# Kernel optimization log

Hardware: AMD Instinct MI355X
Metric: run time of the kernel (lower is better)

Reference implementation:

```python
import jax, jax.numpy as jnp
import numpy as np

B, S, H, NH = 2, 2048, 2048, 16
HD = H // NH  # 128
ROPE_BASE = 10000.0


def _rope(q, k, position_ids):
    # q, k: [B, NH, S, HD]; position_ids: [B, S]
    half = HD // 2
    inv_freq = 1.0 / (ROPE_BASE ** (jnp.arange(0, half, dtype=jnp.float32) / half))
    freqs = position_ids.astype(jnp.float32)[:, :, None] * inv_freq[None, None, :]  # [B,S,half]
    emb = jnp.concatenate([freqs, freqs], axis=-1)                                   # [B,S,HD]
    cos = jnp.cos(emb)[:, None, :, :]  # [B,1,S,HD]
    sin = jnp.sin(emb)[:, None, :, :]

    def rot_half(x):
        x1, x2 = jnp.split(x, 2, axis=-1)
        return jnp.concatenate([-x2, x1], axis=-1)

    q = q * cos + rot_half(q) * sin
    k = k * cos + rot_half(k) * sin
    return q, k


def setup_inputs() -> dict:
    key = jax.random.key(0)
    k1, k2, k3 = jax.random.split(key, 3)
    hidden_states = jax.random.normal(k1, (B, S, H), dtype=jnp.float32)
    position_ids = jnp.broadcast_to(jnp.arange(S, dtype=jnp.int32), (B, S))
    # additive causal mask (large finite negative to avoid inf arithmetic)
    causal = jnp.triu(jnp.full((S, S), -1e9, dtype=jnp.float32), k=1)
    attention_mask = jnp.broadcast_to(causal[None, None], (B, 1, S, S))
    qkv_w = jax.random.normal(k2, (3 * H, H), dtype=jnp.float32) * (H ** -0.5)
    qkv_b = jnp.zeros((3 * H,), dtype=jnp.float32)
    o_w = jax.random.normal(k3, (H, H), dtype=jnp.float32) * (H ** -0.5)
    return {"hidden_states": hidden_states, "position_ids": position_ids,
            "attention_mask": attention_mask, "qkv_w": qkv_w, "qkv_b": qkv_b, "o_w": o_w}


def reference(hidden_states, position_ids, attention_mask, qkv_w, qkv_b, o_w):
    qkv = hidden_states @ qkv_w.T + qkv_b                      # [B,S,3H]
    q, k, v = jnp.split(qkv, 3, axis=-1)

    def to_heads(x):
        return x.reshape(B, S, NH, HD).transpose(0, 2, 1, 3)   # [B,NH,S,HD]

    q, k, v = to_heads(q), to_heads(k), to_heads(v)
    q, k = _rope(q, k, position_ids)

    scale = 1.0 / np.sqrt(HD)
    scores = jnp.einsum('bhqd,bhkd->bhqk', q, k * scale)
    scores = scores + attention_mask
    probs = jax.nn.softmax(scores.astype(jnp.float32), axis=-1).astype(q.dtype)
    attn = jnp.einsum('bhqk,bhkd->bhqd', probs, v)
    attn = attn.transpose(0, 2, 1, 3).reshape(B, S, H)
    return attn @ o_w.T
```

## Files before the change

kernel.cpp:

```cpp
#include <hip/hip_runtime.h>
#include <hip/hip_bf16.h>

#define BB 2
#define SS 2048
#define HH 2048
#define NHH 16
#define HDD 128

using f32x4  = __attribute__((ext_vector_type(4))) float;
using bf16x8 = __attribute__((ext_vector_type(8))) short;

__device__ __forceinline__ unsigned short f2bf(float x) {
  unsigned int u = __float_as_uint(x);
  unsigned int r = (u + 0x7FFFu + ((u >> 16) & 1u)) >> 16;
  return (unsigned short)r;
}
__device__ __forceinline__ float bf2f(unsigned short u) {
  return __uint_as_float(((unsigned int)u) << 16);
}

__device__ __forceinline__ void gll16(const void* g, void* l) {
  __builtin_amdgcn_global_load_lds(
      (__attribute__((address_space(1))) void*)(g),
      (__attribute__((address_space(3))) void*)(l), 16, 0, 0);
}

#define MFMA16(a, b, c) __builtin_amdgcn_mfma_f32_16x16x32_bf16(a, b, c, 0, 0, 0)


__global__ void convert_bf16(const float* __restrict__ in, unsigned short* __restrict__ out, int n4) {
  int i = blockIdx.x * blockDim.x + threadIdx.x;
  if (i >= n4) return;
  float4 v = reinterpret_cast<const float4*>(in)[i];
  ushort4 o;
  o.x = f2bf(v.x); o.y = f2bf(v.y); o.z = f2bf(v.z); o.w = f2bf(v.w);
  reinterpret_cast<ushort4*>(out)[i] = o;
}

__global__ void build_tab(float* __restrict__ tab) {
  int i = blockIdx.x * blockDim.x + threadIdx.x;
  if (i >= SS * 64) return;
  int s = i >> 6, j = i & 63;
  float invf = expf(-logf(10000.f) * ((float)j / 64.f));
  float a = (float)s * invf;
  tab[i * 2]     = cosf(a);
  tab[i * 2 + 1] = sinf(a);
}


template<int MODE, int MI>
__global__ __launch_bounds__(512, 1)
void gemm_pipe(const unsigned short* __restrict__ A,
               const unsigned short* __restrict__ Bw,
               const float* __restrict__ bias,
               float* __restrict__ outF,
               unsigned short* __restrict__ outQ,
               unsigned short* __restrict__ outK,
               unsigned short* __restrict__ outV,
               int Kdim) {
  constexpr int BM = 32 * MI;
  __shared__ unsigned short lA[2][BM * 64];
  __shared__ unsigned short lB[2][256 * 64];
  const int tid = threadIdx.x;
  const int tn = blockIdx.x, tm = blockIdx.y;
  const int wid = tid >> 6, lane = tid & 63;
  const int wm = wid >> 2, wn = wid & 3;
  const int lr = lane & 15, lg = lane >> 4;

  const unsigned short* Ab = A + (size_t)tm * BM * Kdim;
  const unsigned short* Bb = Bw + (size_t)tn * 256 * Kdim;

  f32x4 acc[MI][4] = {};
  bf16x8 af[MI][2], bfr[4][2];

  const int nt = Kdim >> 6;

  auto stageA = [&](int t, int h) {
    unsigned short* L = lA[t & 1];
    const int k0 = t << 6;
#pragma unroll
    for (int p = 0; p < BM / 128; ++p) {
      int cl = p * 512 + tid;
      int ri = cl >> 3, c = cl & 7;
      int row = (ri / (8 * MI)) * (16 * MI) + h * (8 * MI) + (ri % (8 * MI));
      int cg = c ^ (row & 7);
      gll16(Ab + (size_t)row * Kdim + k0 + (cg << 3), L + row * 64 + (c << 3));
    }
  };
  auto stageB = [&](int t, int h) {
    unsigned short* L = lB[t & 1];
    const int k0 = t << 6;
#pragma unroll
    for (int p = 0; p < 2; ++p) {
      int cl = p * 512 + tid;
      int ri = cl >> 3, c = cl & 7;
      int row = (ri >> 5 << 6) + (h << 5) + (ri & 31);
      int cg = c ^ (row & 7);
      gll16(Bb + (size_t)row * Kdim + k0 + (cg << 3), L + row * 64 + (c << 3));
    }
  };
  auto readAhalf = [&](int g, int h) {
    const unsigned short* la = lA[g & 1];
#pragma unroll
    for (int mi = h * (MI / 2); mi < (h + 1) * (MI / 2); ++mi) {
      int ra = wm * (BM / 2) + mi * 16 + lr;
      af[mi][0] = *reinterpret_cast<const bf16x8*>(la + ra * 64 + ((lg ^ (ra & 7)) << 3));
      af[mi][1] = *reinterpret_cast<const bf16x8*>(la + ra * 64 + (((4 + lg) ^ (ra & 7)) << 3));
    }
  };
  auto readBhalf = [&](int g, int h) {
    const unsigned short* lb = lB[g & 1];
#pragma unroll
    for (int ni = h * 2; ni < h * 2 + 2; ++ni) {
      int rb = wn * 64 + ni * 16 + lr;
      bfr[ni][0] = *reinterpret_cast<const bf16x8*>(lb + rb * 64 + ((lg ^ (rb & 7)) << 3));
      bfr[ni][1] = *reinterpret_cast<const bf16x8*>(lb + rb * 64 + (((4 + lg) ^ (rb & 7)) << 3));
    }
  };
  auto quad = [&](int ah, int bh) {
    __builtin_amdgcn_s_setprio(1);
#pragma unroll
    for (int mi = ah * (MI / 2); mi < (ah + 1) * (MI / 2); ++mi)
#pragma unroll
      for (int ni = bh * 2; ni < bh * 2 + 2; ++ni) {
        acc[mi][ni] = MFMA16(af[mi][0], bfr[ni][0], acc[mi][ni]);
        acc[mi][ni] = MFMA16(af[mi][1], bfr[ni][1], acc[mi][ni]);
      }
    __builtin_amdgcn_s_setprio(0);
  };

  stageA(0, 0); stageA(0, 1); stageB(0, 0); stageB(0, 1);
  stageA(1, 0); stageA(1, 1); stageB(1, 0); stageB(1, 1);
  if constexpr (MI == 8) asm volatile("s_waitcnt vmcnt(8)" ::: "memory");
  else                   asm volatile("s_waitcnt vmcnt(6)" ::: "memory");
  __builtin_amdgcn_s_barrier();
  __builtin_amdgcn_sched_barrier(0);
  readAhalf(0, 0);
  readBhalf(0, 0);

  for (int g = 0; g < nt; ++g) {
    readBhalf(g, 1);
    asm volatile("s_waitcnt lgkmcnt(4)" ::: "memory");
    __builtin_amdgcn_sched_barrier(0);
    quad(0, 0);

    readAhalf(g, 1);
    if constexpr (MI == 8) asm volatile("s_waitcnt lgkmcnt(8)" ::: "memory");
    else                   asm volatile("s_waitcnt lgkmcnt(4)" ::: "memory");
    __builtin_amdgcn_sched_barrier(0);
    quad(0, 1);

    asm volatile("s_waitcnt vmcnt(0) lgkmcnt(0)" ::: "memory");
    __builtin_amdgcn_s_barrier();
    __builtin_amdgcn_sched_barrier(0);
    if (g + 1 < nt) readAhalf(g + 1, 0);
    if (g + 2 < nt) { stageA(g + 2, 0); stageA(g + 2, 1); }
    quad(1, 0);

    if (g + 1 < nt) readBhalf(g + 1, 0);
    if (g + 2 < nt) { stageB(g + 2, 0); stageB(g + 2, 1); }
    quad(1, 1);
  }

#pragma unroll
  for (int mi = 0; mi < MI; ++mi) {
#pragma unroll
    for (int ni = 0; ni < 4; ++ni) {
      int n = tn * 256 + wn * 64 + ni * 16 + lr;
#pragma unroll
      for (int r = 0; r < 4; ++r) {
        int m = tm * BM + wm * (BM / 2) + mi * 16 + lg * 4 + r;
        float v = acc[mi][ni][r];
        if (MODE == 1) {
          v += bias[n];
          int sel = n >> 11;
          int h = (n >> 7) & 15;
          int d = n & 127;
          int b = m >> 11;
          int s = m & 2047;
          if (sel == 0)
            outQ[(((size_t)(b * 16 + h)) * 2048 + s) * 128 + d] = f2bf(v);
          else if (sel == 1)
            outK[(((size_t)(b * 16 + h)) * 2048 + s) * 128 + d] = f2bf(v);
          else
            outV[(((size_t)(b * 16 + h)) * 128 + d) * 2048 + s] = f2bf(v);
        } else {
          outF[(size_t)m * 2048 + n] = v;
        }
      }
    }
  }
}


__global__ void rope_inplace(unsigned short* __restrict__ Qr, unsigned short* __restrict__ Kr,
                             const int* __restrict__ pos, const float* __restrict__ tab) {
  int i = blockIdx.x * blockDim.x + threadIdx.x;
  if (i >= (1 << 20)) return;
  int jb = i & 7;
  int s  = (i >> 3) & 2047;
  int bh = (i >> 14) & 31;
  int a  = i >> 19;
  unsigned short* base = (a ? Kr : Qr) + (((size_t)bh * 2048 + s) * 128);
  int b = bh >> 4;
  int p = pos[b * 2048 + s];
  bf16x8 x1 = *reinterpret_cast<bf16x8*>(base + jb * 8);
  bf16x8 x2 = *reinterpret_cast<bf16x8*>(base + 64 + jb * 8);
  bf16x8 y1, y2;
#pragma unroll
  for (int t = 0; t < 8; ++t) {
    int j = jb * 8 + t;
    float c  = tab[((size_t)p * 64 + j) * 2];
    float sn = tab[((size_t)p * 64 + j) * 2 + 1];
    float a1 = bf2f((unsigned short)x1[t]);
    float a2 = bf2f((unsigned short)x2[t]);
    y1[t] = (short)f2bf(a1 * c - a2 * sn);
    y2[t] = (short)f2bf(a2 * c + a1 * sn);
  }
  *reinterpret_cast<bf16x8*>(base + jb * 8) = y1;
  *reinterpret_cast<bf16x8*>(base + 64 + jb * 8) = y2;
}


__global__ __launch_bounds__(256)
void attn_fwd(const unsigned short* __restrict__ Qr,
              const unsigned short* __restrict__ Kr,
              const unsigned short* __restrict__ Vt,
              unsigned short* __restrict__ attnb) {
  __shared__ unsigned short Ks[64 * 128];
  __shared__ unsigned short Vs[128 * 64];
  __shared__ unsigned short Ps[64 * 64];
  const int bx = blockIdx.x, bh = blockIdx.y;
  const int tid = threadIdx.x;
  const int wid = tid >> 6, lane = tid & 63;
  const int lr = lane & 15, lg = lane >> 4;
  const unsigned short* Qb = Qr + (size_t)bh * SS * HDD;
  const unsigned short* Kb = Kr + (size_t)bh * SS * HDD;
  const unsigned short* Vb = Vt + (size_t)bh * HDD * SS;
  const int b = bh >> 4, h = bh & 15;

#pragma unroll 1
  for (int qi = 0; qi < 2; ++qi) {
    const int qt = qi ? bx : (31 - bx);

    bf16x8 qf[4];
#pragma unroll
    for (int kk = 0; kk < 4; ++kk)
      qf[kk] = *reinterpret_cast<const bf16x8*>(
          Qb + ((size_t)(qt * 64 + wid * 16 + lr)) * 128 + kk * 32 + lg * 8);

    f32x4 oacc[8] = {};
    float mrow[4], lsum[4];
#pragma unroll
    for (int r = 0; r < 4; ++r) { mrow[r] = -1e30f; lsum[r] = 0.f; }

    for (int kt = 0; kt <= qt; ++kt) {
#pragma unroll
      for (int ch = 0; ch < 4; ++ch) {
        int c = tid + ch * 256;
        {
          int row = c >> 4, cb = c & 15;
          gll16(Kb + ((size_t)(kt * 64 + row)) * 128 + ((cb ^ (row & 7)) << 3), Ks + c * 8);
        }
        {
          int row = c >> 3, cb = c & 7;
          gll16(Vb + (size_t)row * SS + kt * 64 + ((cb ^ (row & 7)) << 3), Vs + c * 8);
        }
      }
      __syncthreads();

      float sv[4][4];
#pragma unroll
      for (int nt = 0; nt < 4; ++nt) {
        f32x4 sa = {};
#pragma unroll
        for (int kk = 0; kk < 4; ++kk) {
          int row = nt * 16 + lr;
          bf16x8 kf = *reinterpret_cast<const bf16x8*>(
              Ks + row * 128 + (((kk * 4 + lg) ^ (row & 7)) << 3));
          sa = __builtin_amdgcn_mfma_f32_16x16x32_bf16(qf[kk], kf, sa, 0, 0, 0);
        }
#pragma unroll
        for (int r = 0; r < 4; ++r) {
          float s = sa[r] * 0.088388347648318447f;
          if (kt == qt && (nt * 16 + lr) > (wid * 16 + lg * 4 + r)) s -= 1e9f;
          sv[nt][r] = s;
        }
      }

      float tmax[4];
#pragma unroll
      for (int r = 0; r < 4; ++r)
        tmax[r] = fmaxf(fmaxf(sv[0][r], sv[1][r]), fmaxf(sv[2][r], sv[3][r]));
#pragma unroll
      for (int r = 0; r < 4; ++r) {
        tmax[r] = fmaxf(tmax[r], __shfl_xor(tmax[r], 1));
        tmax[r] = fmaxf(tmax[r], __shfl_xor(tmax[r], 2));
        tmax[r] = fmaxf(tmax[r], __shfl_xor(tmax[r], 4));
        tmax[r] = fmaxf(tmax[r], __shfl_xor(tmax[r], 8));
      }
      float fr[4], tsum[4];
#pragma unroll
      for (int r = 0; r < 4; ++r) {
        float mn = fmaxf(mrow[r], tmax[r]);
        fr[r] = __expf(mrow[r] - mn);
        mrow[r] = mn;
        tsum[r] = 0.f;
      }
#pragma unroll
      for (int nt = 0; nt < 4; ++nt) {
        int colc = nt * 2 + (lr >> 3);
#pragma unroll
        for (int r = 0; r < 4; ++r) {
          float p = __expf(sv[nt][r] - mrow[r]);
          tsum[r] += p;
          int row = wid * 16 + lg * 4 + r;
          Ps[row * 64 + ((colc ^ (row & 7)) << 3) + (lr & 7)] = f2bf(p);
        }
      }
#pragma unroll
      for (int r = 0; r < 4; ++r) {
        tsum[r] += __shfl_xor(tsum[r], 1);
        tsum[r] += __shfl_xor(tsum[r], 2);
        tsum[r] += __shfl_xor(tsum[r], 4);
        tsum[r] += __shfl_xor(tsum[r], 8);
        lsum[r] = lsum[r] * fr[r] + tsum[r];
      }
#pragma unroll
      for (int ct = 0; ct < 8; ++ct)
#pragma unroll
        for (int r = 0; r < 4; ++r)
          oacc[ct][r] *= fr[r];

      bf16x8 pf[2];
#pragma unroll
      for (int ks = 0; ks < 2; ++ks) {
        int row = wid * 16 + lr;
        pf[ks] = *reinterpret_cast<const bf16x8*>(
            Ps + row * 64 + (((ks * 4 + lg) ^ (row & 7)) << 3));
      }
#pragma unroll
      for (int ct = 0; ct < 8; ++ct) {
#pragma unroll
        for (int ks = 0; ks < 2; ++ks) {
          int row = ct * 16 + lr;
          bf16x8 vf = *reinterpret_cast<const bf16x8*>(
              Vs + row * 64 + (((ks * 4 + lg) ^ (row & 7)) << 3));
          oacc[ct] = __builtin_amdgcn_mfma_f32_16x16x32_bf16(pf[ks], vf, oacc[ct], 0, 0, 0);
        }
      }
      __syncthreads();
    }

#pragma unroll
    for (int r = 0; r < 4; ++r) {
      float rl = 1.f / lsum[r];
      int qg = qt * 64 + wid * 16 + lg * 4 + r;
#pragma unroll
      for (int ct = 0; ct < 8; ++ct) {
        int d = ct * 16 + lr;
        attnb[((size_t)b * SS + qg) * HH + h * 128 + d] = f2bf(oacc[ct][r] * rl);
      }
    }
  }
}


extern "C" void kernel_launch(void* const* d_in, const int* in_sizes, int n_in,
                              void* d_out, int out_size, void* d_ws, size_t ws_size,
                              hipStream_t stream) {
  const float* hs     = (const float*)d_in[0];
  const int*   pos    = (const int*)d_in[1];
  const float* qkv_w  = (const float*)d_in[3];
  const float* qkv_b  = (const float*)d_in[4];
  const float* o_w    = (const float*)d_in[5];
  float* out = (float*)d_out;
  char* ws = (char*)d_ws;

  unsigned short* hsb   = (unsigned short*)(ws);
  unsigned short* wqkvb = (unsigned short*)(ws + 16777216);
  unsigned short* owb   = (unsigned short*)(ws + 41943040);
  unsigned short* Qr    = (unsigned short*)(ws + 50331648);
  unsigned short* Kr    = (unsigned short*)(ws + 67108864);
  unsigned short* Vt    = (unsigned short*)(ws + 83886080);
  unsigned short* attnb = (unsigned short*)(ws + 100663296);
  float*          tab   = (float*)(ws + 117440512);

  convert_bf16<<<2097152 / 256, 256, 0, stream>>>(hs, hsb, 2097152);
  convert_bf16<<<3145728 / 256, 256, 0, stream>>>(qkv_w, wqkvb, 3145728);
  convert_bf16<<<1048576 / 256, 256, 0, stream>>>(o_w, owb, 1048576);
  build_tab<<<512, 256, 0, stream>>>(tab);

  gemm_pipe<1, 8><<<dim3(24, 16), 512, 0, stream>>>(hsb, wqkvb, qkv_b, nullptr, Qr, Kr, Vt, 2048);
  rope_inplace<<<4096, 256, 0, stream>>>(Qr, Kr, pos, tab);
  attn_fwd<<<dim3(16, 32), 256, 0, stream>>>(Qr, Kr, Vt, attnb);
  gemm_pipe<0, 4><<<dim3(8, 32), 512, 0, stream>>>(attnb, owb, nullptr, out, nullptr, nullptr, nullptr, 2048);
}
```

Measured before the change: 318.7 us.

## Parametrize GEMM N-tile width and double-buffer K/V tiles in attention

The GEMM kernel gains an NB template parameter so the QKV projection can use 192-wide N tiles. That gives 32x16=512 blocks instead of 24x16=384, which should fill the CUs more evenly; the wait counts and the MFMA/read interleave are regenerated per column fragment. The attention kernel now double-buffers its K and V LDS tiles, issuing the next tile's global-to-LDS loads before computing on the current one, with explicit vmcnt waits and raw barriers in place of __syncthreads. This doubles the attention kernel's K/V LDS footprint, and the hand-tuned waitcnt values depend on the exact number of loads issued per thread.

```diff
diff --git a/kernel.cpp b/kernel.cpp
--- a/kernel.cpp
+++ b/kernel.cpp
@@ -26,6 +26,26 @@
 }
 
 #define MFMA16(a, b, c) __builtin_amdgcn_mfma_f32_16x16x32_bf16(a, b, c, 0, 0, 0)
+
+template<int N> __device__ __forceinline__ void wlgkm() {
+  static_assert(N == 0 || N == 2 || N == 4 || N == 6 || N == 8 || N == 10 || N == 12,
+                "unsupported lgkmcnt");
+  if constexpr (N == 0)       asm volatile("s_waitcnt lgkmcnt(0)"  ::: "memory");
+  else if constexpr (N == 2)  asm volatile("s_waitcnt lgkmcnt(2)"  ::: "memory");
+  else if constexpr (N == 4)  asm volatile("s_waitcnt lgkmcnt(4)"  ::: "memory");
+  else if constexpr (N == 6)  asm volatile("s_waitcnt lgkmcnt(6)"  ::: "memory");
+  else if constexpr (N == 8)  asm volatile("s_waitcnt lgkmcnt(8)"  ::: "memory");
+  else if constexpr (N == 10) asm volatile("s_waitcnt lgkmcnt(10)" ::: "memory");
+  else if constexpr (N == 12) asm volatile("s_waitcnt lgkmcnt(12)" ::: "memory");
+}
+template<int N> __device__ __forceinline__ void wvm() {
+  static_assert(N == 0 || N == 5 || N == 6 || N == 7 || N == 8, "unsupported vmcnt");
+  if constexpr (N == 0)      asm volatile("s_waitcnt vmcnt(0)" ::: "memory");
+  else if constexpr (N == 5) asm volatile("s_waitcnt vmcnt(5)" ::: "memory");
+  else if constexpr (N == 6) asm volatile("s_waitcnt vmcnt(6)" ::: "memory");
+  else if constexpr (N == 7) asm volatile("s_waitcnt vmcnt(7)" ::: "memory");
+  else if constexpr (N == 8) asm volatile("s_waitcnt vmcnt(8)" ::: "memory");
+}
 
 
 __global__ void convert_bf16(const float* __restrict__ in, unsigned short* __restrict__ out, int n4) {
@@ -48,7 +68,7 @@
 }
 
 
-template<int MODE, int MI>
+template<int MODE, int MI, int NB>
 __global__ __launch_bounds__(512, 1)
 void gemm_pipe(const unsigned short* __restrict__ A,
                const unsigned short* __restrict__ Bw,
@@ -59,8 +79,10 @@
                unsigned short* __restrict__ outV,
                int Kdim) {
   constexpr int BM = 32 * MI;
+  constexpr int BN = 64 * NB;
+  constexpr int TOPS = 2 * (BM / 128) + NB;
   __shared__ unsigned short lA[2][BM * 64];
-  __shared__ unsigned short lB[2][256 * 64];
+  __shared__ unsigned short lB[2][BN * 64];
   const int tid = threadIdx.x;
   const int tn = blockIdx.x, tm = blockIdx.y;
   const int wid = tid >> 6, lane = tid & 63;
@@ -68,10 +90,10 @@
   const int lr = lane & 15, lg = lane >> 4;
 
   const unsigned short* Ab = A + (size_t)tm * BM * Kdim;
-  const unsigned short* Bb = Bw + (size_t)tn * 256 * Kdim;
-
-  f32x4 acc[MI][4] = {};
-  bf16x8 af[MI][2], bfr[4][2];
+  const unsigned short* Bb = Bw + (size_t)tn * BN * Kdim;
+
+  f32x4 acc[MI][NB] = {};
+  bf16x8 af[MI][2], bfr[NB][2];
 
   const int nt = Kdim >> 6;
 
@@ -90,14 +112,11 @@
   auto stageB = [&](int t, int h) {
     unsigned short* L = lB[t & 1];
     const int k0 = t << 6;
-#pragma unroll
-    for (int p = 0; p < 2; ++p) {
-      int cl = p * 512 + tid;
-      int ri = cl >> 3, c = cl & 7;
-      int row = (ri >> 5 << 6) + (h << 5) + (ri & 31);
-      int cg = c ^ (row & 7);
-      gll16(Bb + (size_t)row * Kdim + k0 + (cg << 3), L + row * 64 + (c << 3));
-    }
+    int cl = tid;
+    int ri = cl >> 3, c = cl & 7;
+    int row = (ri >> 4) * (16 * NB) + h * 16 + (ri & 15);
+    int cg = c ^ (row & 7);
+    gll16(Bb + (size_t)row * Kdim + k0 + (cg << 3), L + row * 64 + (c << 3));
   };
   auto readAhalf = [&](int g, int h) {
     const unsigned short* la = lA[g & 1];
@@ -108,47 +127,55 @@
       af[mi][1] = *reinterpret_cast<const bf16x8*>(la + ra * 64 + (((4 + lg) ^ (ra & 7)) << 3));
     }
   };
-  auto readBhalf = [&](int g, int h) {
+  auto readB = [&](int g, int ni) {
     const unsigned short* lb = lB[g & 1];
-#pragma unroll
-    for (int ni = h * 2; ni < h * 2 + 2; ++ni) {
-      int rb = wn * 64 + ni * 16 + lr;
-      bfr[ni][0] = *reinterpret_cast<const bf16x8*>(lb + rb * 64 + ((lg ^ (rb & 7)) << 3));
-      bfr[ni][1] = *reinterpret_cast<const bf16x8*>(lb + rb * 64 + (((4 + lg) ^ (rb & 7)) << 3));
-    }
-  };
-  auto quad = [&](int ah, int bh) {
+    int rb = wn * (16 * NB) + ni * 16 + lr;
+    bfr[ni][0] = *reinterpret_cast<const bf16x8*>(lb + rb * 64 + ((lg ^ (rb & 7)) << 3));
+    bfr[ni][1] = *reinterpret_cast<const bf16x8*>(lb + rb * 64 + (((4 + lg) ^ (rb & 7)) << 3));
+  };
+  auto quad = [&](int ah, int ni) {
     __builtin_amdgcn_s_setprio(1);
 #pragma unroll
-    for (int mi = ah * (MI / 2); mi < (ah + 1) * (MI / 2); ++mi)
-#pragma unroll
-      for (int ni = bh * 2; ni < bh * 2 + 2; ++ni) {
-        acc[mi][ni] = MFMA16(af[mi][0], bfr[ni][0], acc[mi][ni]);
-        acc[mi][ni] = MFMA16(af[mi][1], bfr[ni][1], acc[mi][ni]);
-      }
+    for (int mi = ah * (MI / 2); mi < (ah + 1) * (MI / 2); ++mi) {
+      acc[mi][ni] = MFMA16(af[mi][0], bfr[ni][0], acc[mi][ni]);
+      acc[mi][ni] = MFMA16(af[mi][1], bfr[ni][1], acc[mi][ni]);
+    }
     __builtin_amdgcn_s_setprio(0);
   };
 
-  stageA(0, 0); stageA(0, 1); stageB(0, 0); stageB(0, 1);
-  stageA(1, 0); stageA(1, 1); stageB(1, 0); stageB(1, 1);
-  if constexpr (MI == 8) asm volatile("s_waitcnt vmcnt(8)" ::: "memory");
-  else                   asm volatile("s_waitcnt vmcnt(6)" ::: "memory");
+  stageA(0, 0); stageA(0, 1);
+#pragma unroll
+  for (int h = 0; h < NB; ++h) stageB(0, h);
+  stageA(1, 0); stageA(1, 1);
+#pragma unroll
+  for (int h = 0; h < NB; ++h) stageB(1, h);
+  wvm<TOPS>();
   __builtin_amdgcn_s_barrier();
   __builtin_amdgcn_sched_barrier(0);
   readAhalf(0, 0);
-  readBhalf(0, 0);
+#pragma unroll
+  for (int ni = 0; ni < NB - 1; ++ni) readB(0, ni);
 
   for (int g = 0; g < nt; ++g) {
-    readBhalf(g, 1);
-    asm volatile("s_waitcnt lgkmcnt(4)" ::: "memory");
+    readB(g, NB - 1);
+    wlgkm<2 * (NB - 1)>();
     __builtin_amdgcn_sched_barrier(0);
     quad(0, 0);
 
     readAhalf(g, 1);
-    if constexpr (MI == 8) asm volatile("s_waitcnt lgkmcnt(8)" ::: "memory");
-    else                   asm volatile("s_waitcnt lgkmcnt(4)" ::: "memory");
+    wlgkm<2 * (NB - 2) + MI>();
     __builtin_amdgcn_sched_barrier(0);
     quad(0, 1);
+
+    if constexpr (NB == 4) {
+      wlgkm<2 + MI>();
+      __builtin_amdgcn_sched_barrier(0);
+      quad(0, 2);
+    }
+
+    wlgkm<MI>();
+    __builtin_amdgcn_sched_barrier(0);
+    quad(0, NB - 1);
 
     asm volatile("s_waitcnt vmcnt(0) lgkmcnt(0)" ::: "memory");
     __builtin_amdgcn_s_barrier();
@@ -157,16 +184,26 @@
     if (g + 2 < nt) { stageA(g + 2, 0); stageA(g + 2, 1); }
     quad(1, 0);
 
-    if (g + 1 < nt) readBhalf(g + 1, 0);
-    if (g + 2 < nt) { stageB(g + 2, 0); stageB(g + 2, 1); }
+    if (g + 1 < nt) readB(g + 1, 0);
+    if (g + 2 < nt) {
+#pragma unroll
+      for (int h = 0; h < NB; ++h) stageB(g + 2, h);
+    }
     quad(1, 1);
+
+    if (g + 1 < nt) readB(g + 1, 1);
+    quad(1, 2);
+    if constexpr (NB == 4) {
+      if (g + 1 < nt) readB(g + 1, 2);
+      quad(1, 3);
+    }
   }
 
 #pragma unroll
   for (int mi = 0; mi < MI; ++mi) {
 #pragma unroll
-    for (int ni = 0; ni < 4; ++ni) {
-      int n = tn * 256 + wn * 64 + ni * 16 + lr;
+    for (int ni = 0; ni < NB; ++ni) {
+      int n = tn * BN + wn * (16 * NB) + ni * 16 + lr;
 #pragma unroll
       for (int r = 0; r < 4; ++r) {
         int m = tm * BM + wm * (BM / 2) + mi * 16 + lg * 4 + r;
@@ -227,8 +264,8 @@
               const unsigned short* __restrict__ Kr,
               const unsigned short* __restrict__ Vt,
               unsigned short* __restrict__ attnb) {
-  __shared__ unsigned short Ks[64 * 128];
-  __shared__ unsigned short Vs[128 * 64];
+  __shared__ unsigned short Ks[2][64 * 128];
+  __shared__ unsigned short Vs[2][128 * 64];
   __shared__ unsigned short Ps[64 * 64];
   const int bx = blockIdx.x, bh = blockIdx.y;
   const int tid = threadIdx.x;
@@ -239,6 +276,21 @@
   const unsigned short* Vb = Vt + (size_t)bh * HDD * SS;
   const int b = bh >> 4, h = bh & 15;
 
+  auto stage = [&](int kt, int buf) {
+#pragma unroll
+    for (int ch = 0; ch < 4; ++ch) {
+      int c = tid + ch * 256;
+      {
+        int row = c >> 4, cb = c & 15;
+        gll16(Kb + ((size_t)(kt * 64 + row)) * 128 + ((cb ^ (row & 7)) << 3), Ks[buf] + c * 8);
+      }
+      {
+        int row = c >> 3, cb = c & 7;
+        gll16(Vb + (size_t)row * SS + kt * 64 + ((cb ^ (row & 7)) << 3), Vs[buf] + c * 8);
+      }
+    }
+  };
+
 #pragma unroll 1
   for (int qi = 0; qi < 2; ++qi) {
     const int qt = qi ? bx : (31 - bx);
@@ -254,20 +306,19 @@
 #pragma unroll
     for (int r = 0; r < 4; ++r) { mrow[r] = -1e30f; lsum[r] = 0.f; }
 
+    int cur = 0;
+    stage(0, 0);
+
+#pragma unroll 1
     for (int kt = 0; kt <= qt; ++kt) {
-#pragma unroll
-      for (int ch = 0; ch < 4; ++ch) {
-        int c = tid + ch * 256;
-        {
-          int row = c >> 4, cb = c & 15;
-          gll16(Kb + ((size_t)(kt * 64 + row)) * 128 + ((cb ^ (row & 7)) << 3), Ks + c * 8);
-        }
-        {
-          int row = c >> 3, cb = c & 7;
-          gll16(Vb + (size_t)row * SS + kt * 64 + ((cb ^ (row & 7)) << 3), Vs + c * 8);
-        }
-      }
-      __syncthreads();
+      if (kt < qt) {
+        stage(kt + 1, cur ^ 1);
+        asm volatile("s_waitcnt vmcnt(8)" ::: "memory");
+      } else {
+        asm volatile("s_waitcnt vmcnt(0)" ::: "memory");
+      }
+      __builtin_amdgcn_s_barrier();
+      __builtin_amdgcn_sched_barrier(0);
 
       float sv[4][4];
 #pragma unroll
@@ -277,7 +328,7 @@
         for (int kk = 0; kk < 4; ++kk) {
           int row = nt * 16 + lr;
           bf16x8 kf = *reinterpret_cast<const bf16x8*>(
-              Ks + row * 128 + (((kk * 4 + lg) ^ (row & 7)) << 3));
+              Ks[cur] + row * 128 + (((kk * 4 + lg) ^ (row & 7)) << 3));
           sa = __builtin_amdgcn_mfma_f32_16x16x32_bf16(qf[kk], kf, sa, 0, 0, 0);
         }
 #pragma unroll
@@ -345,11 +396,12 @@
         for (int ks = 0; ks < 2; ++ks) {
           int row = ct * 16 + lr;
           bf16x8 vf = *reinterpret_cast<const bf16x8*>(
-              Vs + row * 64 + (((ks * 4 + lg) ^ (row & 7)) << 3));
+              Vs[cur] + row * 64 + (((ks * 4 + lg) ^ (row & 7)) << 3));
           oacc[ct] = __builtin_amdgcn_mfma_f32_16x16x32_bf16(pf[ks], vf, oacc[ct], 0, 0, 0);
         }
       }
-      __syncthreads();
+      __builtin_amdgcn_s_barrier();
+      cur ^= 1;
     }
 
 #pragma unroll
@@ -391,8 +443,8 @@
   convert_bf16<<<1048576 / 256, 256, 0, stream>>>(o_w, owb, 1048576);
   build_tab<<<512, 256, 0, stream>>>(tab);
 
-  gemm_pipe<1, 8><<<dim3(24, 16), 512, 0, stream>>>(hsb, wqkvb, qkv_b, nullptr, Qr, Kr, Vt, 2048);
+  gemm_pipe<1, 8, 3><<<dim3(32, 16), 512, 0, stream>>>(hsb, wqkvb, qkv_b, nullptr, Qr, Kr, Vt, 2048);
   rope_inplace<<<4096, 256, 0, stream>>>(Qr, Kr, pos, tab);
   attn_fwd<<<dim3(16, 32), 256, 0, stream>>>(Qr, Kr, Vt, attnb);
-  gemm_pipe<0, 4><<<dim3(8, 32), 512, 0, stream>>>(attnb, owb, nullptr, out, nullptr, nullptr, nullptr, 2048);
-}
+  gemm_pipe<0, 4, 4><<<dim3(8, 32), 512, 0, stream>>>(attnb, owb, nullptr, out, nullptr, nullptr, nullptr, 2048);
+}
```

Result: no change. 318.1 us (-0.2%).
